# Kernel optimization log

Hardware: AMD Instinct MI355X
Metric: run time of the kernel (lower is better)

Reference implementation:

```python
import jax, jax.numpy as jnp
import numpy as np

PATCH = 96
STRIDE = PATCH // 2  # 48


def setup_inputs() -> dict:
    key = jax.random.key(0)
    kx = jax.random.fold_in(key, 0)
    x = jax.random.uniform(kx, (8, 4, 1056, 1056), dtype=jnp.float32)
    mu_pristine = jnp.zeros((36,), dtype=jnp.float32)
    cov_pristine = jnp.eye(36, dtype=jnp.float32)
    return {"x": x, "mu_pristine": mu_pristine, "cov_pristine": cov_pristine}


def _extract_patches(x):
    # x: [B, C, H, W] -> overlapping patches [B, C, N, P, P], stride = P//2
    B, C, H, W = x.shape
    nH = (H - PATCH) // STRIDE + 1
    nW = (W - PATCH) // STRIDE + 1
    idx_h = np.arange(nH)[:, None] * STRIDE + np.arange(PATCH)[None, :]  # [nH, P]
    idx_w = np.arange(nW)[:, None] * STRIDE + np.arange(PATCH)[None, :]  # [nW, P]
    p = x[:, :, idx_h, :]            # [B, C, nH, P, W]
    p = p[:, :, :, :, idx_w]         # [B, C, nH, P, nW, P]
    p = p.transpose(0, 1, 2, 4, 3, 5)  # [B, C, nH, nW, P, P]
    return p.reshape(B, C, nH * nW, PATCH, PATCH)


def reference(x, mu_pristine, cov_pristine):
    patches = _extract_patches(x)  # [B, C, N, P, P]
    mu = patches.mean(axis=(-2, -1))                    # [B, C, N]
    var = patches.var(axis=(-2, -1), ddof=1)            # unbiased, matches torch.var
    gx = jnp.diff(patches, axis=-1)                     # [B, C, N, P, P-1]
    gy = jnp.diff(patches, axis=-2)                     # [B, C, N, P-1, P]
    grad_mag = jnp.sqrt((gx * gx).mean(axis=(-2, -1)) + (gy * gy).mean(axis=(-2, -1)))
    # torch concatenates [mu, var, grad_mag] along channel dim per patch, then means over patches
    feats = jnp.concatenate([mu, var, grad_mag], axis=1).mean(axis=-1)  # [B, 3C]
    d = feats.shape[1]
    mu0 = mu_pristine[:d]
    cov_inv = jnp.linalg.inv(cov_pristine[:d, :d])
    diff = feats - mu0[None, :]
    dist = jnp.sqrt(((diff @ cov_inv) * diff).sum(axis=1))  # Mahalanobis distance [B]
    return dist.mean()
```

## Files before the change

### kernel.cpp

```cpp
#include <hip/hip_runtime.h>
#include <math.h>

#define PATCH 96
#define STRIDE 48
#define NH 21
#define NW 21
#define NP (NH * NW)
#define BATCH 8
#define CHAN 4
#define NBC (BATCH * CHAN)
#define IMG_H 1056
#define IMG_W 1056
#define NHB 44
#define NCHUNK 22
#define NSTAT 6
#define NPIX 9216.0f
#define NGRAD 9120.0f

__global__ __launch_bounds__(320) void band_stats_kernel(
    const float* __restrict__ x, float* __restrict__ pf) {
  __shared__ float acc[NCHUNK * NSTAT];

  const int t = threadIdx.x;
  const int bc = blockIdx.x / NHB;
  const int hb = blockIdx.x - bc * NHB;
  const bool active = t < 264;
  const int tc = active ? t : 263;
  const int noff = (tc == 263) ? 3 : 4;

  const float* rowbase = x + (size_t)bc * (IMG_H * IMG_W)
                           + (size_t)(hb * 24) * IMG_W
                           + (size_t)(4 * tc);

  float s1 = 0.f, s2 = 0.f, gxi = 0.f, gxb = 0.f, gyi = 0.f, gyb = 0.f;
  const bool bnd_is_gxb = ((tc % 12) == 11);

#define SUMS_GX(A, nxt)                                                  \
  do {                                                                   \
    s1 += (A).x + (A).y + (A).z + (A).w;                                 \
    s2 += (A).x * (A).x + (A).y * (A).y + (A).z * (A).z + (A).w * (A).w; \
    float d1 = (A).y - (A).x, d2 = (A).z - (A).y, d3 = (A).w - (A).z;    \
    float d4 = (nxt) - (A).w;                                            \
    gxi += d1 * d1 + d2 * d2 + d3 * d3;                                  \
    float bd = d4 * d4;                                                  \
    if (bnd_is_gxb) gxb += bd; else gxi += bd;                           \
  } while (0)

  float4 prev;
  {
    const float4 A = *(const float4*)rowbase;
    const float nxt = rowbase[noff];
    SUMS_GX(A, nxt);
    prev = A;
  }
#pragma unroll 4
  for (int r = 1; r < 24; ++r) {
    const float4 A = *(const float4*)(rowbase + (size_t)r * IMG_W);
    const float nxt = rowbase[(size_t)r * IMG_W + noff];
    SUMS_GX(A, nxt);
    const float e0 = A.x - prev.x, e1 = A.y - prev.y,
                e2 = A.z - prev.z, e3 = A.w - prev.w;
    gyi += e0 * e0 + e1 * e1 + e2 * e2 + e3 * e3;
    prev = A;
  }
  if (hb != NHB - 1) {
    const float4 A = *(const float4*)(rowbase + (size_t)24 * IMG_W);
    const float e0 = A.x - prev.x, e1 = A.y - prev.y,
                e2 = A.z - prev.z, e3 = A.w - prev.w;
    gyb = e0 * e0 + e1 * e1 + e2 * e2 + e3 * e3;
  }
#undef SUMS_GX

  for (int i = t; i < NCHUNK * NSTAT; i += 320) acc[i] = 0.f;
  __syncthreads();
  if (active) {
    const int chunk = tc / 12;
    atomicAdd(&acc[chunk * NSTAT + 0], s1);
    atomicAdd(&acc[chunk * NSTAT + 1], s2);
    atomicAdd(&acc[chunk * NSTAT + 2], gxi);
    atomicAdd(&acc[chunk * NSTAT + 3], gxb);
    atomicAdd(&acc[chunk * NSTAT + 4], gyi);
    atomicAdd(&acc[chunk * NSTAT + 5], gyb);
  }
  __syncthreads();
  float* dst = pf + (size_t)(bc * NHB + hb) * (NCHUNK * NSTAT);
  for (int i = t; i < NCHUNK * NSTAT; i += 320) dst[i] = acc[i];
}

__global__ __launch_bounds__(512) void patch_feats_kernel(
    const float* __restrict__ pf, float* __restrict__ featsG) {
  __shared__ float S[NHB * NCHUNK * NSTAT];
  __shared__ float wsum[8][3];

  const int bc = blockIdx.x;
  const int t = threadIdx.x;
  const float* src = pf + (size_t)bc * (NHB * NCHUNK * NSTAT);
  for (int i = t; i < NHB * NCHUNK * NSTAT; i += 512) S[i] = src[i];
  __syncthreads();

  float fmu = 0.f, fvar = 0.f, fg = 0.f;
  if (t < NP) {
    const int ph = t / NW, pw = t - ph * NW;
    const int h0 = 2 * ph;
#define AT(h, c, s) S[((h) * NCHUNK + (c)) * NSTAT + (s)]
    float S1 = 0.f, S2 = 0.f, Gx = 0.f, Gy = 0.f;
#pragma unroll
    for (int hh = 0; hh < 4; ++hh) {
      const int h = h0 + hh;
      S1 += AT(h, pw, 0) + AT(h, pw + 1, 0);
      S2 += AT(h, pw, 1) + AT(h, pw + 1, 1);
      Gx += AT(h, pw, 2) + AT(h, pw, 3) + AT(h, pw + 1, 2);
      Gy += AT(h, pw, 4) + AT(h, pw + 1, 4);
    }
#pragma unroll
    for (int hh = 0; hh < 3; ++hh) {
      const int h = h0 + hh;
      Gy += AT(h, pw, 5) + AT(h, pw + 1, 5);
    }
#undef AT
    fmu = S1 / NPIX;
    fvar = (S2 - S1 * S1 / NPIX) / (NPIX - 1.f);
    fg = sqrtf((Gx + Gy) / NGRAD);
  }
#pragma unroll
  for (int off = 32; off > 0; off >>= 1) {
    fmu += __shfl_xor(fmu, off);
    fvar += __shfl_xor(fvar, off);
    fg += __shfl_xor(fg, off);
  }
  const int wave = t >> 6;
  if ((t & 63) == 0) { wsum[wave][0] = fmu; wsum[wave][1] = fvar; wsum[wave][2] = fg; }
  __syncthreads();
  if (t == 0) {
    float m = 0.f, v = 0.f, g = 0.f;
#pragma unroll
    for (int w = 0; w < 8; ++w) { m += wsum[w][0]; v += wsum[w][1]; g += wsum[w][2]; }
    const int b = bc / CHAN, c = bc - b * CHAN;
    featsG[b * 12 + 0 + c] = m / (float)NP;
    featsG[b * 12 + 4 + c] = v / (float)NP;
    featsG[b * 12 + 8 + c] = g / (float)NP;
  }
}

__global__ __launch_bounds__(64) void finalize_kernel(
    const float* __restrict__ featsG, const float* __restrict__ mu0_full,
    const float* __restrict__ cov_full, float* __restrict__ out) {
  __shared__ float feats_s[96];
  __shared__ double inv_s[12][12];
  __shared__ float dist[BATCH];

  const int t = threadIdx.x;
  feats_s[t] = featsG[t];
  if (t < 32) feats_s[64 + t] = featsG[64 + t];

  double M[12];
#pragma unroll
  for (int r = 0; r < 12; ++r) {
    double v = 0.0;
    if (t < 12) v = (double)cov_full[r * 36 + t];
    else if (t < 24) v = (t - 12 == r) ? 1.0 : 0.0;
    M[r] = v;
  }

#pragma unroll
  for (int k = 0; k < 12; ++k) {
    const double piv = __shfl(M[k], k);
    const double ip = 1.0 / piv;
    M[k] *= ip;
#pragma unroll
    for (int r = 0; r < 12; ++r) {
      if (r == k) continue;
      const double f = __shfl(M[r], k);
      M[r] -= f * M[k];
    }
  }

  if (t >= 12 && t < 24) {
    const int j = t - 12;
#pragma unroll
    for (int r = 0; r < 12; ++r) inv_s[r][j] = M[r];
  }
  __syncthreads();

  if (t < BATCH) {
    double acc = 0.0;
    double d[12];
#pragma unroll
    for (int i = 0; i < 12; ++i)
      d[i] = (double)feats_s[t * 12 + i] - (double)mu0_full[i];
#pragma unroll
    for (int i = 0; i < 12; ++i) {
      double row = 0.0;
#pragma unroll
      for (int j = 0; j < 12; ++j) row += inv_s[i][j] * d[j];
      acc += d[i] * row;
    }
    dist[t] = (float)sqrt(acc);
  }
  __syncthreads();
  if (t == 0) {
    float m = 0.f;
#pragma unroll
    for (int b = 0; b < BATCH; ++b) m += dist[b];
    out[0] = m / (float)BATCH;
  }
}

extern "C" void kernel_launch(void* const* d_in, const int* in_sizes, int n_in,
                              void* d_out, int out_size, void* d_ws, size_t ws_size,
                              hipStream_t stream) {
  const float* x   = (const float*)d_in[0];
  const float* mu0 = (const float*)d_in[1];
  const float* cov = (const float*)d_in[2];
  float* out = (float*)d_out;
  float* pf     = (float*)d_ws;
  float* featsG = pf + (size_t)NBC * NHB * NCHUNK * NSTAT;

  band_stats_kernel<<<NBC * NHB, 320, 0, stream>>>(x, pf);
  patch_feats_kernel<<<NBC, 512, 0, stream>>>(pf, featsG);
  finalize_kernel<<<1, 64, 0, stream>>>(featsG, mu0, cov, out);
}
```

Before: 225.9 us.

## Fuse three kernels into one using last-block-done atomic tickets

Merges the band-stats, patch-feature and finalize kernels into a single launch. The last block to finish each (b,c) slab, found through an atomic counter, computes the patch features, and the last of those computes the Mahalanobis distance. This removes two kernel launches and their inter-kernel gaps. In exchange it adds a memset launch, threadfences, atomics, and a larger shared-memory footprint (about 23KB slab) that may reduce occupancy of the bandwidth-bound stats phase.

```diff
diff --git a/kernel.cpp b/kernel.cpp
--- a/kernel.cpp
+++ b/kernel.cpp
@@ -16,14 +16,23 @@
 #define NSTAT 6
 #define NPIX 9216.0f
 #define NGRAD 9120.0f
-
-__global__ __launch_bounds__(320) void band_stats_kernel(
-    const float* __restrict__ x, float* __restrict__ pf) {
-  __shared__ float acc[NCHUNK * NSTAT];
+#define SLAB (NHB * NCHUNK * NSTAT)
+
+__global__ __launch_bounds__(320, 5) void fused_kernel(
+    const float* __restrict__ x, float* __restrict__ pf,
+    float* __restrict__ featsG, int* __restrict__ cnt,
+    const float* __restrict__ mu0_full, const float* __restrict__ cov_full,
+    float* __restrict__ out) {
+  __shared__ float S[SLAB];
+  __shared__ float wsum[5][3];
+  __shared__ double inv_s[12][12];
+  __shared__ float fin_s[96 + BATCH];
+  __shared__ int ticket_s;
 
   const int t = threadIdx.x;
   const int bc = blockIdx.x / NHB;
   const int hb = blockIdx.x - bc * NHB;
+
   const bool active = t < 264;
   const int tc = active ? t : 263;
   const int noff = (tc == 263) ? 3 : 4;
@@ -71,38 +80,43 @@
   }
 #undef SUMS_GX
 
-  for (int i = t; i < NCHUNK * NSTAT; i += 320) acc[i] = 0.f;
+  for (int i = t; i < NCHUNK * NSTAT; i += 320) S[i] = 0.f;
   __syncthreads();
   if (active) {
     const int chunk = tc / 12;
-    atomicAdd(&acc[chunk * NSTAT + 0], s1);
-    atomicAdd(&acc[chunk * NSTAT + 1], s2);
-    atomicAdd(&acc[chunk * NSTAT + 2], gxi);
-    atomicAdd(&acc[chunk * NSTAT + 3], gxb);
-    atomicAdd(&acc[chunk * NSTAT + 4], gyi);
-    atomicAdd(&acc[chunk * NSTAT + 5], gyb);
-  }
-  __syncthreads();
-  float* dst = pf + (size_t)(bc * NHB + hb) * (NCHUNK * NSTAT);
-  for (int i = t; i < NCHUNK * NSTAT; i += 320) dst[i] = acc[i];
-}
-
-__global__ __launch_bounds__(512) void patch_feats_kernel(
-    const float* __restrict__ pf, float* __restrict__ featsG) {
-  __shared__ float S[NHB * NCHUNK * NSTAT];
-  __shared__ float wsum[8][3];
-
-  const int bc = blockIdx.x;
-  const int t = threadIdx.x;
-  const float* src = pf + (size_t)bc * (NHB * NCHUNK * NSTAT);
-  for (int i = t; i < NHB * NCHUNK * NSTAT; i += 512) S[i] = src[i];
-  __syncthreads();
-
-  float fmu = 0.f, fvar = 0.f, fg = 0.f;
-  if (t < NP) {
-    const int ph = t / NW, pw = t - ph * NW;
+    atomicAdd(&S[chunk * NSTAT + 0], s1);
+    atomicAdd(&S[chunk * NSTAT + 1], s2);
+    atomicAdd(&S[chunk * NSTAT + 2], gxi);
+    atomicAdd(&S[chunk * NSTAT + 3], gxb);
+    atomicAdd(&S[chunk * NSTAT + 4], gyi);
+    atomicAdd(&S[chunk * NSTAT + 5], gyb);
+  }
+  __syncthreads();
+
+  if (t < 64) {
+    float* dst = pf + (size_t)(bc * NHB + hb) * (NCHUNK * NSTAT);
+    for (int i = t; i < NCHUNK * NSTAT; i += 64) dst[i] = S[i];
+    __threadfence();
+  }
+  __syncthreads();
+  if (t == 0) ticket_s = atomicAdd(&cnt[bc], 1);
+  __syncthreads();
+  if (ticket_s != NHB - 1) return;
+
+  __threadfence();
+  {
+    const float* src = pf + (size_t)bc * SLAB;
+    for (int i = t; i < SLAB; i += 320)
+      S[i] = __hip_atomic_load(&src[i], __ATOMIC_RELAXED,
+                               __HIP_MEMORY_SCOPE_AGENT);
+  }
+  __syncthreads();
+
+  float am = 0.f, av = 0.f, ag = 0.f;
+#define AT(h, c, s) S[((h) * NCHUNK + (c)) * NSTAT + (s)]
+  for (int p = t; p < NP; p += 320) {
+    const int ph = p / NW, pw = p - ph * NW;
     const int h0 = 2 * ph;
-#define AT(h, c, s) S[((h) * NCHUNK + (c)) * NSTAT + (s)]
     float S1 = 0.f, S2 = 0.f, Gx = 0.f, Gy = 0.f;
 #pragma unroll
     for (int hh = 0; hh < 4; ++hh) {
@@ -117,68 +131,66 @@
       const int h = h0 + hh;
       Gy += AT(h, pw, 5) + AT(h, pw + 1, 5);
     }
+    am += S1 / NPIX;
+    av += (S2 - S1 * S1 / NPIX) / (NPIX - 1.f);
+    ag += sqrtf((Gx + Gy) / NGRAD);
+  }
 #undef AT
-    fmu = S1 / NPIX;
-    fvar = (S2 - S1 * S1 / NPIX) / (NPIX - 1.f);
-    fg = sqrtf((Gx + Gy) / NGRAD);
-  }
 #pragma unroll
   for (int off = 32; off > 0; off >>= 1) {
-    fmu += __shfl_xor(fmu, off);
-    fvar += __shfl_xor(fvar, off);
-    fg += __shfl_xor(fg, off);
+    am += __shfl_xor(am, off);
+    av += __shfl_xor(av, off);
+    ag += __shfl_xor(ag, off);
   }
   const int wave = t >> 6;
-  if ((t & 63) == 0) { wsum[wave][0] = fmu; wsum[wave][1] = fvar; wsum[wave][2] = fg; }
+  if ((t & 63) == 0) { wsum[wave][0] = am; wsum[wave][1] = av; wsum[wave][2] = ag; }
   __syncthreads();
   if (t == 0) {
     float m = 0.f, v = 0.f, g = 0.f;
 #pragma unroll
-    for (int w = 0; w < 8; ++w) { m += wsum[w][0]; v += wsum[w][1]; g += wsum[w][2]; }
+    for (int w = 0; w < 5; ++w) { m += wsum[w][0]; v += wsum[w][1]; g += wsum[w][2]; }
     const int b = bc / CHAN, c = bc - b * CHAN;
     featsG[b * 12 + 0 + c] = m / (float)NP;
     featsG[b * 12 + 4 + c] = v / (float)NP;
     featsG[b * 12 + 8 + c] = g / (float)NP;
-  }
-}
-
-__global__ __launch_bounds__(64) void finalize_kernel(
-    const float* __restrict__ featsG, const float* __restrict__ mu0_full,
-    const float* __restrict__ cov_full, float* __restrict__ out) {
-  __shared__ float feats_s[96];
-  __shared__ double inv_s[12][12];
-  __shared__ float dist[BATCH];
-
-  const int t = threadIdx.x;
-  feats_s[t] = featsG[t];
-  if (t < 32) feats_s[64 + t] = featsG[64 + t];
-
-  double M[12];
-#pragma unroll
-  for (int r = 0; r < 12; ++r) {
-    double v = 0.0;
-    if (t < 12) v = (double)cov_full[r * 36 + t];
-    else if (t < 24) v = (t - 12 == r) ? 1.0 : 0.0;
-    M[r] = v;
-  }
-
-#pragma unroll
-  for (int k = 0; k < 12; ++k) {
-    const double piv = __shfl(M[k], k);
-    const double ip = 1.0 / piv;
-    M[k] *= ip;
+    __threadfence();
+    ticket_s = atomicAdd(&cnt[NBC], 1);
+  }
+  __syncthreads();
+  if (ticket_s != NBC - 1) return;
+
+  __threadfence();
+  if (t < 96)
+    fin_s[t] = __hip_atomic_load(&featsG[t], __ATOMIC_RELAXED,
+                                 __HIP_MEMORY_SCOPE_AGENT);
+  __syncthreads();
+
+  if (t < 64) {
+    double M[12];
 #pragma unroll
     for (int r = 0; r < 12; ++r) {
-      if (r == k) continue;
-      const double f = __shfl(M[r], k);
-      M[r] -= f * M[k];
-    }
-  }
-
-  if (t >= 12 && t < 24) {
-    const int j = t - 12;
-#pragma unroll
-    for (int r = 0; r < 12; ++r) inv_s[r][j] = M[r];
+      double v = 0.0;
+      if (t < 12) v = (double)cov_full[r * 36 + t];
+      else if (t < 24) v = (t - 12 == r) ? 1.0 : 0.0;
+      M[r] = v;
+    }
+#pragma unroll
+    for (int k = 0; k < 12; ++k) {
+      const double piv = __shfl(M[k], k);
+      const double ip = 1.0 / piv;
+      M[k] *= ip;
+#pragma unroll
+      for (int r = 0; r < 12; ++r) {
+        if (r == k) continue;
+        const double f = __shfl(M[r], k);
+        M[r] -= f * M[k];
+      }
+    }
+    if (t >= 12 && t < 24) {
+      const int j = t - 12;
+#pragma unroll
+      for (int r = 0; r < 12; ++r) inv_s[r][j] = M[r];
+    }
   }
   __syncthreads();
 
@@ -187,7 +199,7 @@
     double d[12];
 #pragma unroll
     for (int i = 0; i < 12; ++i)
-      d[i] = (double)feats_s[t * 12 + i] - (double)mu0_full[i];
+      d[i] = (double)fin_s[t * 12 + i] - (double)mu0_full[i];
 #pragma unroll
     for (int i = 0; i < 12; ++i) {
       double row = 0.0;
@@ -195,13 +207,13 @@
       for (int j = 0; j < 12; ++j) row += inv_s[i][j] * d[j];
       acc += d[i] * row;
     }
-    dist[t] = (float)sqrt(acc);
+    fin_s[96 + t] = (float)sqrt(acc);
   }
   __syncthreads();
   if (t == 0) {
     float m = 0.f;
 #pragma unroll
-    for (int b = 0; b < BATCH; ++b) m += dist[b];
+    for (int b = 0; b < BATCH; ++b) m += fin_s[96 + b];
     out[0] = m / (float)BATCH;
   }
 }
@@ -214,9 +226,9 @@
   const float* cov = (const float*)d_in[2];
   float* out = (float*)d_out;
   float* pf     = (float*)d_ws;
-  float* featsG = pf + (size_t)NBC * NHB * NCHUNK * NSTAT;
-
-  band_stats_kernel<<<NBC * NHB, 320, 0, stream>>>(x, pf);
-  patch_feats_kernel<<<NBC, 512, 0, stream>>>(pf, featsG);
-  finalize_kernel<<<1, 64, 0, stream>>>(featsG, mu0, cov, out);
+  float* featsG = pf + (size_t)NBC * SLAB;
+  int* cnt      = (int*)(featsG + 96);
+
+  hipMemsetAsync(cnt, 0, (NBC + 1) * sizeof(int), stream);
+  fused_kernel<<<NBC * NHB, 320, 0, stream>>>(x, pf, featsG, cnt, mu0, cov, out);
 }
```

Result: slower. 301.9 us (+33.6%).
